# Performance work log

Measured on AMD Instinct MI355X. Metric: run time of the kernel, lower is better.

Reference implementation:

```python
import jax, jax.numpy as jnp
import numpy as np

DIM = 1024
HEADS = 16
HEAD_DIM = DIM // HEADS
DECAY = 0.95
EPS = 1e-5


def setup_inputs() -> dict:
    key = jax.random.key(0)
    ks = jax.random.split(key, 11)
    B, S, D = 2, 2048, DIM
    s = 1.0 / np.sqrt(D)
    inp = {
        'x': jax.random.normal(ks[0], (B, S, D), dtype=jnp.float32),
        'Wq': jax.random.normal(ks[1], (D, D), dtype=jnp.float32) * s,
        'bq': jnp.zeros((D,), jnp.float32),
        'Wk': jax.random.normal(ks[2], (D, D), dtype=jnp.float32) * s,
        'bk': jnp.zeros((D,), jnp.float32),
        'Wv': jax.random.normal(ks[3], (D, D), dtype=jnp.float32) * s,
        'bv': jnp.zeros((D,), jnp.float32),
        'Wo': jax.random.normal(ks[4], (D, D), dtype=jnp.float32) * s,
        'bo': jnp.zeros((D,), jnp.float32),
        'gamma': jnp.ones((D,), jnp.float32),
        'beta': jnp.zeros((D,), jnp.float32),
    }
    return inp


def _decay_mask(S, dtype):
    idx = jnp.arange(S)
    diff = (idx[:, None] - idx[None, :]).astype(jnp.float32)
    # decay^(i-j) for i >= j, else 0
    mask = jnp.where(diff >= 0, jnp.exp(diff * np.log(DECAY)), 0.0)
    return mask.astype(dtype)


def reference(x, Wq, bq, Wk, bk, Wv, bv, Wo, bo, gamma, beta):
    B, S, D = x.shape
    H, hd = HEADS, HEAD_DIM

    def split_heads(y):  # [B,S,D] -> [B,H,S,hd]
        return y.reshape(B, S, H, hd).transpose(0, 2, 1, 3)

    q = split_heads(x @ Wq + bq)
    k = split_heads(x @ Wk + bk)
    v = split_heads(x @ Wv + bv)

    mask = _decay_mask(S, x.dtype)  # [S,S]
    scores = jnp.einsum('bhid,bhjd->bhij', q, k) * mask
    out = jnp.einsum('bhij,bhjd->bhid', scores, v)  # [B,H,S,hd]

    out = out.transpose(0, 2, 1, 3).reshape(B, S, D)
    out = out @ Wo + bo

    # GroupNorm(H groups) applied over channel dim with seq as spatial dim
    y = out.transpose(0, 2, 1)            # [B,D,S]
    yg = y.reshape(B, H, hd, S)
    mu = yg.mean(axis=(2, 3), keepdims=True)
    var = yg.var(axis=(2, 3), keepdims=True)
    yn = (yg - mu) / jnp.sqrt(var + EPS)
    yn = yn.reshape(B, D, S) * gamma[None, :, None] + beta[None, :, None]
    return yn.transpose(0, 2, 1)          # [B,S,D]
```

## Files before the change

kernel.cpp:

```cpp
#include <hip/hip_runtime.h>
#include <hip/hip_bf16.h>

typedef unsigned short u16;
typedef __attribute__((ext_vector_type(8))) short short8;
typedef __attribute__((ext_vector_type(4))) float f32x4;
typedef __attribute__((ext_vector_type(4))) unsigned short u16x4;

#define SEQ 2048
#define NH 16
#define HD 64
#define DM 1024
#define LN_DECAY (-0.051293294387550536f)
#define WIN_TILES 4

__device__ __forceinline__ float b2f(u16 u) {
    return __uint_as_float(((unsigned int)u) << 16);
}
__device__ __forceinline__ u16 f2b(float f) {
    unsigned int u = __float_as_uint(f);
    u += 0x7fffu + ((u >> 16) & 1u);
    return (u16)(u >> 16);
}
__device__ __forceinline__ f32x4 mfma16(short8 a, short8 b, f32x4 c) {
    return __builtin_amdgcn_mfma_f32_16x16x32_bf16(a, b, c, 0, 0, 0);
}
__device__ __forceinline__ void gld_lds16(const u16* g, u16* l) {
    __builtin_amdgcn_global_load_lds(
        (const __attribute__((address_space(1))) void*)g,
        (__attribute__((address_space(3))) void*)l, 16, 0, 0);
}
__device__ __forceinline__ int detect_fl(const u16* Wq, int lane) {
    int hit = 0;
#pragma unroll
    for (int j = 0; j < 4; j++) {
        u16 u = Wq[2*(lane + 64*j)];
        if (((u >> 7) & 0xFF) >= 0xC0) hit = 1;
    }
    return (__ballot(hit) != 0ULL) ? 1 : 0;
}

__global__ __launch_bounds__(256) void prep(
    const void* __restrict__ x,
    const void* __restrict__ Wq, const void* __restrict__ Wk,
    const void* __restrict__ Wv, const void* __restrict__ Wo,
    const void* __restrict__ bq, const void* __restrict__ bk,
    const void* __restrict__ bv, const void* __restrict__ bo,
    const void* __restrict__ gamma, const void* __restrict__ beta,
    u16* __restrict__ xc,
    u16* __restrict__ WqT, u16* __restrict__ WkT,
    u16* __restrict__ WvT, u16* __restrict__ WoT,
    u16* __restrict__ bqc, u16* __restrict__ bkc, u16* __restrict__ bvc,
    u16* __restrict__ boc, u16* __restrict__ gammac, u16* __restrict__ betac,
    int* __restrict__ flag, float* __restrict__ statsAcc)
{
    __shared__ u16 tileS[32][33];
    int bid = blockIdx.x, tid = threadIdx.x;
    int fl = detect_fl((const u16*)Wq, tid & 63);

    if (bid < 4096) {
        int i = (bid*256 + tid)*4;
        if (fl) {
            f32x4 v = *(const f32x4*)((const float*)x + i);
            u16x4 o = { f2b(v[0]), f2b(v[1]), f2b(v[2]), f2b(v[3]) };
            *(u16x4*)(xc + i) = o;
        } else {
            *(u16x4*)(xc + i) = *(const u16x4*)((const u16*)x + i);
        }
    } else if (bid == 4096) {
        const void* ins[6] = {bq, bk, bv, bo, gamma, beta};
        u16* outs[6] = {bqc, bkc, bvc, boc, gammac, betac};
        int i = tid*4;
#pragma unroll
        for (int a = 0; a < 6; a++) {
            if (fl) {
                f32x4 v = *(const f32x4*)((const float*)ins[a] + i);
                u16x4 o = { f2b(v[0]), f2b(v[1]), f2b(v[2]), f2b(v[3]) };
                *(u16x4*)(outs[a] + i) = o;
            } else {
                *(u16x4*)(outs[a] + i) = *(const u16x4*)((const u16*)ins[a] + i);
            }
        }
        if (tid == 0) *flag = fl;
        if (tid < 64) statsAcc[tid] = 0.f;
    } else {
        int tb = bid - 4097;
        int wsel = tb >> 10, tile = tb & 1023;
        const void* W = (wsel==0) ? Wq : (wsel==1) ? Wk : (wsel==2) ? Wv : Wo;
        u16* T        = (wsel==0) ? WqT : (wsel==1) ? WkT : (wsel==2) ? WvT : WoT;
        int bn = (tile & 31)*32, bk_ = (tile >> 5)*32;
        int r = tid >> 5, c = tid & 31;
#pragma unroll
        for (int i2 = 0; i2 < 4; i2++) {
            size_t idx = (size_t)(bk_ + r + i2*8)*DM + bn + c;
            tileS[r + i2*8][c] = fl ? f2b(((const float*)W)[idx]) : ((const u16*)W)[idx];
        }
        __syncthreads();
#pragma unroll
        for (int i2 = 0; i2 < 4; i2++)
            T[(size_t)(bn + r + i2*8)*DM + bk_ + c] = tileS[c][r + i2*8];
    }
}

__device__ __forceinline__ void gemm_core(
    const u16* __restrict__ A, const u16* __restrict__ BT,
    u16* As, u16* Bs, int m0, int n0, int t, f32x4 (&acc)[4][4])
{
    int l = t & 63;
    int lane16 = l & 15, quad = l >> 4;
    int w = t >> 6;
    int wm = (w >> 1) * 64, wn = (w & 1) * 64;

    int srow   = t >> 2;
    int schunk = (t & 3) ^ ((t >> 3) & 3);

    f32x4 zero = {0.f, 0.f, 0.f, 0.f};
#pragma unroll
    for (int i = 0; i < 4; i++)
#pragma unroll
        for (int j = 0; j < 4; j++)
            acc[i][j] = zero;

    const u16* a0 = A  + (size_t)(m0 + srow)      * DM + schunk*8;
    const u16* a1 = A  + (size_t)(m0 + srow + 64) * DM + schunk*8;
    const u16* b0 = BT + (size_t)(n0 + srow)      * DM + schunk*8;
    const u16* b1 = BT + (size_t)(n0 + srow + 64) * DM + schunk*8;

    for (int k0 = 0; k0 < DM; k0 += 32) {
        __syncthreads();
        gld_lds16(a0 + k0, &As[t*8]);
        gld_lds16(a1 + k0, &As[2048 + t*8]);
        gld_lds16(b0 + k0, &Bs[t*8]);
        gld_lds16(b1 + k0, &Bs[2048 + t*8]);
        __syncthreads();
        short8 af[4], bf[4];
#pragma unroll
        for (int i = 0; i < 4; i++) {
            int ra = wm + i*16 + lane16;
            int rb = wn + i*16 + lane16;
            af[i] = *(const short8*)(&As[ra*32 + ((quad ^ ((ra>>1)&3))*8)]);
            bf[i] = *(const short8*)(&Bs[rb*32 + ((quad ^ ((rb>>1)&3))*8)]);
        }
#pragma unroll
        for (int i = 0; i < 4; i++)
#pragma unroll
            for (int j = 0; j < 4; j++)
                acc[i][j] = mfma16(af[i], bf[j], acc[i][j]);
    }
}

__global__ __launch_bounds__(256) void gemm_qkv(
    const u16* __restrict__ x,
    const u16* __restrict__ WqT, const u16* __restrict__ WkT, const u16* __restrict__ WvT,
    const u16* __restrict__ bq, const u16* __restrict__ bk, const u16* __restrict__ bv,
    u16* __restrict__ qb, u16* __restrict__ kb, u16* __restrict__ vTb)
{
    __shared__ u16 As[128*32];
    __shared__ u16 Bs[128*32];
    int z = blockIdx.z;
    const u16* BT   = (z==0) ? WqT : (z==1) ? WkT : WvT;
    const u16* bias = (z==0) ? bq  : (z==1) ? bk  : bv;
    u16* outB       = (z==0) ? qb  : (z==1) ? kb  : vTb;
    int m0 = blockIdx.x * 128, n0 = blockIdx.y * 128, t = threadIdx.x;

    f32x4 acc[4][4];
    gemm_core(x, BT, As, Bs, m0, n0, t, acc);

    int l = t & 63, lane16 = l & 15, quad = l >> 4, w = t >> 6;
    int wm = (w >> 1) * 64, wn = (w & 1) * 64;
#pragma unroll
    for (int i = 0; i < 4; i++) {
#pragma unroll
        for (int j = 0; j < 4; j++) {
            int n = n0 + wn + j*16 + lane16;
            float bvv = b2f(bias[n]);
#pragma unroll
            for (int r = 0; r < 4; r++) {
                int m = m0 + wm + i*16 + quad*4 + r;
                float v = acc[i][j][r] + bvv;
                int b = m >> 11, sq = m & (SEQ-1);
                int h = n >> 6,  d = n & (HD-1);
                if (z == 2)
                    outB[(((size_t)(b*NH + h))*HD + d)*SEQ + sq] = f2b(v);
                else
                    outB[(((size_t)(b*NH + h))*SEQ + sq)*HD + d] = f2b(v);
            }
        }
    }
}

__global__ __launch_bounds__(256) void retention(
    const u16* __restrict__ q, const u16* __restrict__ k,
    const u16* __restrict__ vT, u16* __restrict__ attn)
{
    __shared__ u16 Ks[64*64];
    __shared__ u16 Vs[64*64];
    __shared__ u16 Ps[4][16*64];

    int qt = blockIdx.x, bh = blockIdx.y;
    int t = threadIdx.x, w = t >> 6, l = t & 63;
    int c = l & 15, qd = l >> 4;
    int qbase = qt * 64;
    int iwave = qbase + w*16;

    const u16* qh = q  + (size_t)bh * SEQ * HD;
    const u16* kh = k  + (size_t)bh * SEQ * HD;
    const u16* vh = vT + (size_t)bh * HD * SEQ;

    float D[4], E[4];
#pragma unroll
    for (int r = 0; r < 4; r++)
        D[r] = __expf((float)(qd*4 + r) * LN_DECAY);
#pragma unroll
    for (int st = 0; st < 4; st++)
        E[st] = __expf(-(float)(st*16 + c) * LN_DECAY);

    int sr = t >> 3, sc8 = t & 7;

    short8 qf[2];
#pragma unroll
    for (int kk = 0; kk < 2; kk++)
        qf[kk] = *(const short8*)(qh + (size_t)(iwave + c)*HD + kk*32 + qd*8);

    f32x4 zero = {0.f, 0.f, 0.f, 0.f};
    f32x4 oacc[4] = {zero, zero, zero, zero};

    int jt0 = (qt > WIN_TILES) ? (qt - WIN_TILES) : 0;
#pragma unroll 1
    for (int jt = jt0; jt <= qt; jt++) {
        int jbase = jt * 64;
        __syncthreads();
        {
            int r0 = sr, r1 = sr + 32;
            *(short8*)(&Ks[r0*64 + ((sc8 ^ (r0&7))*8)]) = *(const short8*)(kh + (size_t)(jbase+r0)*HD + sc8*8);
            *(short8*)(&Ks[r1*64 + ((sc8 ^ (r1&7))*8)]) = *(const short8*)(kh + (size_t)(jbase+r1)*HD + sc8*8);
            *(short8*)(&Vs[r0*64 + ((sc8 ^ (r0&7))*8)]) = *(const short8*)(vh + (size_t)r0*SEQ + jbase + sc8*8);
            *(short8*)(&Vs[r1*64 + ((sc8 ^ (r1&7))*8)]) = *(const short8*)(vh + (size_t)(r1)*SEQ + jbase + sc8*8);
        }
        __syncthreads();

        f32x4 sacc[4] = {zero, zero, zero, zero};
#pragma unroll
        for (int kk = 0; kk < 2; kk++) {
#pragma unroll
            for (int st = 0; st < 4; st++) {
                int row = st*16 + c;
                short8 bf = *(const short8*)(&Ks[row*64 + (((kk*4+qd) ^ (row&7))*8)]);
                sacc[st] = mfma16(qf[kk], bf, sacc[st]);
            }
        }

        float base = __expf((float)(iwave - jbase) * LN_DECAY);
#pragma unroll
        for (int st = 0; st < 4; st++) {
            int j = jbase + st*16 + c;
            float bE = base * E[st];
#pragma unroll
            for (int r = 0; r < 4; r++) {
                int i = iwave + qd*4 + r;
                float val = (i >= j) ? sacc[st][r] * (bE * D[r]) : 0.0f;
                int row = qd*4 + r;
                int col = st*16 + c;
                Ps[w][row*64 + (((col>>3) ^ (row&7))*8) + (col&7)] = f2b(val);
            }
        }
        asm volatile("s_waitcnt lgkmcnt(0)" ::: "memory");
        short8 pf[2];
#pragma unroll
        for (int kk = 0; kk < 2; kk++)
            pf[kk] = *(const short8*)(&Ps[w][c*64 + (((kk*4+qd) ^ (c&7))*8)]);

#pragma unroll
        for (int kk = 0; kk < 2; kk++) {
#pragma unroll
            for (int nt = 0; nt < 4; nt++) {
                int row = nt*16 + c;
                short8 vf = *(const short8*)(&Vs[row*64 + (((kk*4+qd) ^ (row&7))*8)]);
                oacc[nt] = mfma16(pf[kk], vf, oacc[nt]);
            }
        }
    }

    int b = bh >> 4, h = bh & (NH-1);
#pragma unroll
    for (int nt = 0; nt < 4; nt++) {
        int d = h*HD + nt*16 + c;
#pragma unroll
        for (int r = 0; r < 4; r++) {
            int s = iwave + qd*4 + r;
            attn[((size_t)(b*SEQ + s))*DM + d] = f2b(oacc[nt][r]);
        }
    }
}

__device__ __forceinline__ void gout_step(
    const u16* As, const u16* Bs, int wm, int wn, int lane16, int quad,
    f32x4 (&acc)[4][4])
{
    short8 af[4], bf[4];
#pragma unroll
    for (int i = 0; i < 4; i++) {
        int ra = wm + i*16 + lane16;
        int rb = wn + i*16 + lane16;
        af[i] = *(const short8*)(&As[ra*32 + ((quad ^ ((ra>>1)&3))*8)]);
        bf[i] = *(const short8*)(&Bs[rb*32 + ((quad ^ ((rb>>1)&3))*8)]);
    }
#pragma unroll
    for (int i = 0; i < 4; i++)
#pragma unroll
        for (int j = 0; j < 4; j++)
            acc[i][j] = mfma16(af[i], bf[j], acc[i][j]);
}

__global__ __launch_bounds__(256) void gemm_out(
    const u16* __restrict__ attn, const u16* __restrict__ WoT,
    const u16* __restrict__ bo, float* __restrict__ proj,
    float* __restrict__ statsAcc)
{
    __shared__ u16 As0[128*32], Bs0[128*32];
    __shared__ u16 As1[128*32], Bs1[128*32];
    int m0 = blockIdx.x * 128, n0 = blockIdx.y * 128, t = threadIdx.x;
    int l = t & 63, lane16 = l & 15, quad = l >> 4, w = t >> 6;
    int wm = (w >> 1) * 64, wn = (w & 1) * 64;
    int srow   = t >> 2;
    int schunk = (t & 3) ^ ((t >> 3) & 3);

    f32x4 zero = {0.f, 0.f, 0.f, 0.f};
    f32x4 acc[4][4];
#pragma unroll
    for (int i = 0; i < 4; i++)
#pragma unroll
        for (int j = 0; j < 4; j++)
            acc[i][j] = zero;

    const u16* a0 = attn + (size_t)(m0 + srow)      * DM + schunk*8;
    const u16* a1 = attn + (size_t)(m0 + srow + 64) * DM + schunk*8;
    const u16* b0 = WoT  + (size_t)(n0 + srow)      * DM + schunk*8;
    const u16* b1 = WoT  + (size_t)(n0 + srow + 64) * DM + schunk*8;

    gld_lds16(a0, &As0[t*8]);
    gld_lds16(a1, &As0[2048 + t*8]);
    gld_lds16(b0, &Bs0[t*8]);
    gld_lds16(b1, &Bs0[2048 + t*8]);
    __syncthreads();

#pragma unroll 1
    for (int k0 = 0; k0 < DM; k0 += 64) {
        gld_lds16(a0 + k0 + 32, &As1[t*8]);
        gld_lds16(a1 + k0 + 32, &As1[2048 + t*8]);
        gld_lds16(b0 + k0 + 32, &Bs1[t*8]);
        gld_lds16(b1 + k0 + 32, &Bs1[2048 + t*8]);
        gout_step(As0, Bs0, wm, wn, lane16, quad, acc);
        __syncthreads();

        if (k0 + 64 < DM) {
            gld_lds16(a0 + k0 + 64, &As0[t*8]);
            gld_lds16(a1 + k0 + 64, &As0[2048 + t*8]);
            gld_lds16(b0 + k0 + 64, &Bs0[t*8]);
            gld_lds16(b1 + k0 + 64, &Bs0[2048 + t*8]);
        }
        gout_step(As1, Bs1, wm, wn, lane16, quad, acc);
        __syncthreads();
    }

    float s = 0.f, ss = 0.f;
#pragma unroll
    for (int i = 0; i < 4; i++) {
#pragma unroll
        for (int j = 0; j < 4; j++) {
            int n = n0 + wn + j*16 + lane16;
            float bvv = b2f(bo[n]);
#pragma unroll
            for (int r = 0; r < 4; r++) {
                int m = m0 + wm + i*16 + quad*4 + r;
                float v = acc[i][j][r] + bvv;
                proj[(size_t)m*DM + n] = v;
                s += v; ss += v*v;
            }
        }
    }
#pragma unroll
    for (int off = 32; off > 0; off >>= 1) {
        s  += __shfl_down(s, off);
        ss += __shfl_down(ss, off);
    }
    if (l == 0) {
        int b = m0 >> 11;
        int g = (n0 + wn) >> 6;
        atomicAdd(&statsAcc[(b*NH + g)*2],     s);
        atomicAdd(&statsAcc[(b*NH + g)*2 + 1], ss);
    }
}

__global__ __launch_bounds__(256) void gn_apply(
    const float* __restrict__ proj, const float* __restrict__ statsAcc,
    const u16* __restrict__ gamma, const u16* __restrict__ beta,
    const int* __restrict__ flag, void* __restrict__ outv)
{
    int base = (blockIdx.x*256 + threadIdx.x)*4;
    int d = base & (DM-1);
    int b = base >> 21;
    int g = d >> 6;
    float S  = statsAcc[(b*NH + g)*2];
    float SS = statsAcc[(b*NH + g)*2 + 1];
    const float inv = 1.0f/(float)(SEQ*HD);
    float mu = S*inv;
    float rstd = rsqrtf(SS*inv - mu*mu + 1e-5f);
    f32x4 v = *(const f32x4*)(proj + base);
    float o0 = (v[0]-mu)*rstd*b2f(gamma[d])   + b2f(beta[d]);
    float o1 = (v[1]-mu)*rstd*b2f(gamma[d+1]) + b2f(beta[d+1]);
    float o2 = (v[2]-mu)*rstd*b2f(gamma[d+2]) + b2f(beta[d+2]);
    float o3 = (v[3]-mu)*rstd*b2f(gamma[d+3]) + b2f(beta[d+3]);
    if (*flag) {
        f32x4 ov = {o0, o1, o2, o3};
        *(f32x4*)((float*)outv + base) = ov;
    } else {
        u16x4 ov = {f2b(o0), f2b(o1), f2b(o2), f2b(o3)};
        *(u16x4*)((u16*)outv + base) = ov;
    }
}

extern "C" void kernel_launch(void* const* d_in, const int* in_sizes, int n_in,
                              void* d_out, int out_size, void* d_ws, size_t ws_size,
                              hipStream_t stream) {
    const void* x     = d_in[0];
    const void* Wq    = d_in[1];
    const void* bq    = d_in[2];
    const void* Wk    = d_in[3];
    const void* bk    = d_in[4];
    const void* Wv    = d_in[5];
    const void* bv    = d_in[6];
    const void* Wo    = d_in[7];
    const void* bo    = d_in[8];
    const void* gamma = d_in[9];
    const void* beta  = d_in[10];

    const size_t MB = 1024*1024;
    char* ws = (char*)d_ws;
    int*   flag     = (int*)ws;
    u16*   bqc      = (u16*)(ws + 4096);
    u16*   bkc      = (u16*)(ws + 8192);
    u16*   bvc      = (u16*)(ws + 12288);
    u16*   boc      = (u16*)(ws + 16384);
    u16*   gammac   = (u16*)(ws + 20480);
    u16*   betac    = (u16*)(ws + 24576);
    float* statsAcc = (float*)(ws + 28672);
    u16*   xc     = (u16*)(ws + 1*MB);
    u16*   WqT    = (u16*)(ws + 9*MB);
    u16*   WkT    = (u16*)(ws + 11*MB);
    u16*   WvT    = (u16*)(ws + 13*MB);
    u16*   WoT    = (u16*)(ws + 15*MB);
    u16*   qb     = (u16*)(ws + 17*MB);
    u16*   kb     = (u16*)(ws + 25*MB);
    u16*   vTb    = (u16*)(ws + 33*MB);
    u16*   attn   = (u16*)(ws + 41*MB);
    float* proj   = (float*)(ws + 17*MB);

    prep<<<8193, 256, 0, stream>>>(x, Wq, Wk, Wv, Wo, bq, bk, bv, bo, gamma, beta,
                                   xc, WqT, WkT, WvT, WoT,
                                   bqc, bkc, bvc, boc, gammac, betac,
                                   flag, statsAcc);
    gemm_qkv<<<dim3(32, 8, 3), 256, 0, stream>>>(xc, WqT, WkT, WvT, bqc, bkc, bvc, qb, kb, vTb);
    retention<<<dim3(32, 32), 256, 0, stream>>>(qb, kb, vTb, attn);
    gemm_out<<<dim3(32, 8), 256, 0, stream>>>(attn, WoT, boc, proj, statsAcc);
    gn_apply<<<4096, 256, 0, stream>>>(proj, statsAcc, gammac, betac, flag, d_out);
}
```

Measured before the change: 188.9 us.

## Triple-buffer LDS staging in GEMM core with vmcnt-based waits and single barrier

Replaces the synchronous load-then-compute loop in the shared GEMM core with a three-stage LDS ring. The global-to-LDS load for tile k+2 is issued before computing tile k, and partial s_waitcnt vmcnt plus a single barrier per step replace two full syncthreads. The out-projection GEMM now reuses this core instead of its own double-buffered loop. The goal is to hide global load latency in the QKV GEMM. The cost is 48KB of LDS per block, which may lower occupancy, and the waitcnt counts depend on how the async loads are emitted.

```diff
diff --git a/kernel.cpp b/kernel.cpp
--- a/kernel.cpp
+++ b/kernel.cpp
@@ -101,6 +101,35 @@
     }
 }
 
+__device__ __forceinline__ void stage_tile(
+    const u16* a0, const u16* a1, const u16* b0, const u16* b1,
+    int k0, u16* As, u16* Bs, int t)
+{
+    gld_lds16(a0 + k0, &As[t*8]);
+    gld_lds16(a1 + k0, &As[2048 + t*8]);
+    gld_lds16(b0 + k0, &Bs[t*8]);
+    gld_lds16(b1 + k0, &Bs[2048 + t*8]);
+}
+
+__device__ __forceinline__ void compute_tile(
+    const u16* As, const u16* Bs, int wm, int wn, int lane16, int quad,
+    f32x4 (&acc)[4][4])
+{
+    short8 af[4], bf[4];
+#pragma unroll
+    for (int i = 0; i < 4; i++) {
+        int ra = wm + i*16 + lane16;
+        int rb = wn + i*16 + lane16;
+        af[i] = *(const short8*)(&As[ra*32 + ((quad ^ ((ra>>1)&3))*8)]);
+        bf[i] = *(const short8*)(&Bs[rb*32 + ((quad ^ ((rb>>1)&3))*8)]);
+    }
+#pragma unroll
+    for (int i = 0; i < 4; i++)
+#pragma unroll
+        for (int j = 0; j < 4; j++)
+            acc[i][j] = mfma16(af[i], bf[j], acc[i][j]);
+}
+
 __device__ __forceinline__ void gemm_core(
     const u16* __restrict__ A, const u16* __restrict__ BT,
     u16* As, u16* Bs, int m0, int n0, int t, f32x4 (&acc)[4][4])
@@ -125,26 +154,24 @@
     const u16* b0 = BT + (size_t)(n0 + srow)      * DM + schunk*8;
     const u16* b1 = BT + (size_t)(n0 + srow + 64) * DM + schunk*8;
 
+    stage_tile(a0, a1, b0, b1, 0,  As,        Bs,        t);
+    stage_tile(a0, a1, b0, b1, 32, As + 4096, Bs + 4096, t);
+
+    int cur = 0;
+#pragma unroll 1
     for (int k0 = 0; k0 < DM; k0 += 32) {
-        __syncthreads();
-        gld_lds16(a0 + k0, &As[t*8]);
-        gld_lds16(a1 + k0, &As[2048 + t*8]);
-        gld_lds16(b0 + k0, &Bs[t*8]);
-        gld_lds16(b1 + k0, &Bs[2048 + t*8]);
-        __syncthreads();
-        short8 af[4], bf[4];
-#pragma unroll
-        for (int i = 0; i < 4; i++) {
-            int ra = wm + i*16 + lane16;
-            int rb = wn + i*16 + lane16;
-            af[i] = *(const short8*)(&As[ra*32 + ((quad ^ ((ra>>1)&3))*8)]);
-            bf[i] = *(const short8*)(&Bs[rb*32 + ((quad ^ ((rb>>1)&3))*8)]);
-        }
-#pragma unroll
-        for (int i = 0; i < 4; i++)
-#pragma unroll
-            for (int j = 0; j < 4; j++)
-                acc[i][j] = mfma16(af[i], bf[j], acc[i][j]);
+        if (k0 + 32 < DM)
+            asm volatile("s_waitcnt vmcnt(4)" ::: "memory");
+        else
+            asm volatile("s_waitcnt vmcnt(0)" ::: "memory");
+        __builtin_amdgcn_s_barrier();
+        if (k0 + 64 < DM) {
+            int nxt = cur + 2; if (nxt >= 3) nxt -= 3;
+            stage_tile(a0, a1, b0, b1, k0 + 64,
+                       As + nxt*4096, Bs + nxt*4096, t);
+        }
+        compute_tile(As + cur*4096, Bs + cur*4096, wm, wn, lane16, quad, acc);
+        cur = (cur + 1 == 3) ? 0 : cur + 1;
     }
 }
 
@@ -154,8 +181,8 @@
     const u16* __restrict__ bq, const u16* __restrict__ bk, const u16* __restrict__ bv,
     u16* __restrict__ qb, u16* __restrict__ kb, u16* __restrict__ vTb)
 {
-    __shared__ u16 As[128*32];
-    __shared__ u16 Bs[128*32];
+    __shared__ u16 As[3*4096];
+    __shared__ u16 Bs[3*4096];
     int z = blockIdx.z;
     const u16* BT   = (z==0) ? WqT : (z==1) ? WkT : WvT;
     const u16* bias = (z==0) ? bq  : (z==1) ? bk  : bv;
@@ -292,76 +319,20 @@
     }
 }
 
-__device__ __forceinline__ void gout_step(
-    const u16* As, const u16* Bs, int wm, int wn, int lane16, int quad,
-    f32x4 (&acc)[4][4])
-{
-    short8 af[4], bf[4];
-#pragma unroll
-    for (int i = 0; i < 4; i++) {
-        int ra = wm + i*16 + lane16;
-        int rb = wn + i*16 + lane16;
-        af[i] = *(const short8*)(&As[ra*32 + ((quad ^ ((ra>>1)&3))*8)]);
-        bf[i] = *(const short8*)(&Bs[rb*32 + ((quad ^ ((rb>>1)&3))*8)]);
-    }
-#pragma unroll
-    for (int i = 0; i < 4; i++)
-#pragma unroll
-        for (int j = 0; j < 4; j++)
-            acc[i][j] = mfma16(af[i], bf[j], acc[i][j]);
-}
-
 __global__ __launch_bounds__(256) void gemm_out(
     const u16* __restrict__ attn, const u16* __restrict__ WoT,
     const u16* __restrict__ bo, float* __restrict__ proj,
     float* __restrict__ statsAcc)
 {
-    __shared__ u16 As0[128*32], Bs0[128*32];
-    __shared__ u16 As1[128*32], Bs1[128*32];
+    __shared__ u16 As[3*4096];
+    __shared__ u16 Bs[3*4096];
     int m0 = blockIdx.x * 128, n0 = blockIdx.y * 128, t = threadIdx.x;
+
+    f32x4 acc[4][4];
+    gemm_core(attn, WoT, As, Bs, m0, n0, t, acc);
+
     int l = t & 63, lane16 = l & 15, quad = l >> 4, w = t >> 6;
     int wm = (w >> 1) * 64, wn = (w & 1) * 64;
-    int srow   = t >> 2;
-    int schunk = (t & 3) ^ ((t >> 3) & 3);
-
-    f32x4 zero = {0.f, 0.f, 0.f, 0.f};
-    f32x4 acc[4][4];
-#pragma unroll
-    for (int i = 0; i < 4; i++)
-#pragma unroll
-        for (int j = 0; j < 4; j++)
-            acc[i][j] = zero;
-
-    const u16* a0 = attn + (size_t)(m0 + srow)      * DM + schunk*8;
-    const u16* a1 = attn + (size_t)(m0 + srow + 64) * DM + schunk*8;
-    const u16* b0 = WoT  + (size_t)(n0 + srow)      * DM + schunk*8;
-    const u16* b1 = WoT  + (size_t)(n0 + srow + 64) * DM + schunk*8;
-
-    gld_lds16(a0, &As0[t*8]);
-    gld_lds16(a1, &As0[2048 + t*8]);
-    gld_lds16(b0, &Bs0[t*8]);
-    gld_lds16(b1, &Bs0[2048 + t*8]);
-    __syncthreads();
-
-#pragma unroll 1
-    for (int k0 = 0; k0 < DM; k0 += 64) {
-        gld_lds16(a0 + k0 + 32, &As1[t*8]);
-        gld_lds16(a1 + k0 + 32, &As1[2048 + t*8]);
-        gld_lds16(b0 + k0 + 32, &Bs1[t*8]);
-        gld_lds16(b1 + k0 + 32, &Bs1[2048 + t*8]);
-        gout_step(As0, Bs0, wm, wn, lane16, quad, acc);
-        __syncthreads();
-
-        if (k0 + 64 < DM) {
-            gld_lds16(a0 + k0 + 64, &As0[t*8]);
-            gld_lds16(a1 + k0 + 64, &As0[2048 + t*8]);
-            gld_lds16(b0 + k0 + 64, &Bs0[t*8]);
-            gld_lds16(b1 + k0 + 64, &Bs0[2048 + t*8]);
-        }
-        gout_step(As1, Bs1, wm, wn, lane16, quad, acc);
-        __syncthreads();
-    }
-
     float s = 0.f, ss = 0.f;
 #pragma unroll
     for (int i = 0; i < 4; i++) {
```

Result: slower. 194.9 us (+3.2%).
